# Kernel optimization log

Measured on AMD Instinct MI355X. Metric: run time of the kernel, lower is better.

## Reference

```python
import jax, jax.numpy as jnp
import numpy as np

B, S, DIM, H = 4, 2048, 1024, 16
DEPTH = DIM // H


def setup_inputs() -> dict:
    key = jax.random.key(0)
    ks = jax.random.split(key, 12)
    s = 0.02
    return {
        "Q": jax.random.normal(ks[0], (B, S, DIM), jnp.float32),
        "K": jax.random.normal(ks[1], (B, S, DIM), jnp.float32),
        "V": jax.random.normal(ks[2], (B, S, DIM), jnp.float32),
        "mask": jax.random.randint(ks[3], (B, 1, 1, S), 0, 2).astype(jnp.float32),
        "Wq": jax.random.normal(ks[4], (DIM, DIM), jnp.float32) * s,
        "bq": jnp.zeros((DIM,), jnp.float32),
        "Wk": jax.random.normal(ks[5], (DIM, DIM), jnp.float32) * s,
        "bk": jnp.zeros((DIM,), jnp.float32),
        "Wv": jax.random.normal(ks[6], (DIM, DIM), jnp.float32) * s,
        "bv": jnp.zeros((DIM,), jnp.float32),
        "Wo": jax.random.normal(ks[7], (DIM, DIM), jnp.float32) * s,
        "bo": jnp.zeros((DIM,), jnp.float32),
    }


def _split_heads(x):
    # [B,S,DIM] -> [B,H,S,DEPTH]
    return x.reshape(x.shape[0], x.shape[1], H, DEPTH).transpose(0, 2, 1, 3)


def reference(Q, K, V, mask, Wq, bq, Wk, bk, Wv, bv, Wo, bo):
    q = _split_heads(Q @ Wq + bq)
    k = _split_heads(K @ Wk + bk)
    v = _split_heads(V @ Wv + bv)
    # scaled dot-product attention; note original scales by sqrt(depth) = last dim of K after split
    logits = jnp.einsum("bhqd,bhkd->bhqk", q, k) / jnp.sqrt(jnp.float32(DEPTH))
    logits = logits + mask * -1e9
    attn = jax.nn.softmax(logits, axis=-1)
    ctx = jnp.einsum("bhqk,bhkd->bhqd", attn, v)
    ctx = ctx.transpose(0, 2, 1, 3).reshape(Q.shape[0], Q.shape[1], DIM)
    return ctx @ Wo + bo
```

## Files before the change

### kernel.cpp

```cpp
#include <hip/hip_runtime.h>

typedef short s16x8 __attribute__((ext_vector_type(8)));
typedef short s16x4 __attribute__((ext_vector_type(4)));
typedef float f32x4 __attribute__((ext_vector_type(4)));

#define MFMA32(a, b, c) __builtin_amdgcn_mfma_f32_16x16x32_bf16((a), (b), (c), 0, 0, 0)

#if defined(__HIP_DEVICE_COMPILE__)
#define MFMA16(a, b, c) __builtin_amdgcn_mfma_f32_16x16x16bf16_1k((a), (b), (c), 0, 0, 0)
#else
#define MFMA16(a, b, c) (c)
#endif

__device__ __forceinline__ void stage16(const unsigned short* g, unsigned short* l) {
#if defined(__HIP_DEVICE_COMPILE__)
  __builtin_amdgcn_global_load_lds((const __attribute__((address_space(1))) unsigned int*)g,
                                   (__attribute__((address_space(3))) unsigned int*)l, 16, 0, 0);
#endif
}

__device__ __forceinline__ unsigned short f2b(float f) {
  unsigned int u = __builtin_bit_cast(unsigned int, f);
  unsigned int r = u + 0x7FFFu + ((u >> 16) & 1u);
  return (unsigned short)(r >> 16);
}
__device__ __forceinline__ unsigned int pk2(float a, float b) {
  return (unsigned int)f2b(a) | ((unsigned int)f2b(b) << 16);
}
__device__ __forceinline__ s16x4 mk4(float p0, float p1, float p2, float p3) {
  uint2 u;
  u.x = pk2(p0, p1);
  u.y = pk2(p2, p3);
  return __builtin_bit_cast(s16x4, u);
}
__device__ __forceinline__ float fast_exp2(float x) {
#if defined(__HIP_DEVICE_COMPILE__) && __has_builtin(__builtin_amdgcn_exp2f)
  return __builtin_amdgcn_exp2f(x);
#else
  return exp2f(x);
#endif
}

__global__ void wtrans(const float* __restrict__ W0, const float* __restrict__ W1,
                       const float* __restrict__ W2, const float* __restrict__ W3,
                       unsigned short* __restrict__ T0, unsigned short* __restrict__ T1,
                       unsigned short* __restrict__ T2, unsigned short* __restrict__ T3) {
  const float* W;
  unsigned short* T;
  switch (blockIdx.z) {
    case 0: W = W0; T = T0; break;
    case 1: W = W1; T = T1; break;
    case 2: W = W2; T = T2; break;
    default: W = W3; T = T3; break;
  }
  __shared__ float tile[32][33];
  const int n0 = blockIdx.x << 5;
  const int k0 = blockIdx.y << 5;
  const int tx = threadIdx.x;
  const int ty = threadIdx.y;
#pragma unroll
  for (int j = 0; j < 4; ++j)
    tile[ty + 8 * j][tx] = W[(size_t)(k0 + ty + 8 * j) * 1024 + n0 + tx];
  __syncthreads();
#pragma unroll
  for (int j = 0; j < 4; ++j)
    T[(size_t)(n0 + ty + 8 * j) * 1024 + k0 + tx] = f2b(tile[tx][ty + 8 * j]);
}

template <int MODE>
__global__ __launch_bounds__(256, 2) void gemm_bt(const void* __restrict__ Ain,
                                                  const unsigned short* __restrict__ Bt,
                                                  const float* __restrict__ bias,
                                                  void* __restrict__ Cout, float oscale) {
  __shared__ unsigned short As[128][40];
  __shared__ unsigned short Bs[128][40];
  const int n0 = blockIdx.x * 128;
  const int m0 = blockIdx.y * 128;
  const int tid = threadIdx.x;
  const int srow = tid >> 1;
  const int kc = (tid & 1) << 4;
  const int w = tid >> 6;
  const int lane = tid & 63;
  const int lr = lane & 15;
  const int lg = lane >> 4;
  const int wm = (w >> 1) << 6;
  const int wn = (w & 1) << 6;

  f32x4 acc[4][4];
#pragma unroll
  for (int i = 0; i < 4; ++i)
#pragma unroll
    for (int j = 0; j < 4; ++j) {
      f32x4 z = {0.f, 0.f, 0.f, 0.f};
      acc[i][j] = z;
    }

  const unsigned short* Bp0 = Bt + (size_t)(n0 + srow) * 1024 + kc;

  for (int k0 = 0; k0 < 1024; k0 += 32) {
    if constexpr (MODE != 2) {
      const float* A = (const float*)Ain + (size_t)(m0 + srow) * 1024 + k0 + kc;
      float4 f0 = ((const float4*)A)[0];
      float4 f1 = ((const float4*)A)[1];
      float4 f2 = ((const float4*)A)[2];
      float4 f3 = ((const float4*)A)[3];
      uint4 u0, u1;
      u0.x = pk2(f0.x, f0.y); u0.y = pk2(f0.z, f0.w);
      u0.z = pk2(f1.x, f1.y); u0.w = pk2(f1.z, f1.w);
      u1.x = pk2(f2.x, f2.y); u1.y = pk2(f2.z, f2.w);
      u1.z = pk2(f3.x, f3.y); u1.w = pk2(f3.z, f3.w);
      *(uint4*)&As[srow][kc] = u0;
      *(uint4*)&As[srow][kc + 8] = u1;
    } else {
      const unsigned short* A = (const unsigned short*)Ain + (size_t)(m0 + srow) * 1024 + k0 + kc;
      *(uint4*)&As[srow][kc] = ((const uint4*)A)[0];
      *(uint4*)&As[srow][kc + 8] = ((const uint4*)A)[1];
    }
    {
      const unsigned short* Bp = Bp0 + k0;
      *(uint4*)&Bs[srow][kc] = ((const uint4*)Bp)[0];
      *(uint4*)&Bs[srow][kc + 8] = ((const uint4*)Bp)[1];
    }
    __syncthreads();
    s16x8 af[4], bfr[4];
#pragma unroll
    for (int mt = 0; mt < 4; ++mt) af[mt] = *(const s16x8*)&As[wm + mt * 16 + lr][lg * 8];
#pragma unroll
    for (int nt = 0; nt < 4; ++nt) bfr[nt] = *(const s16x8*)&Bs[wn + nt * 16 + lr][lg * 8];
#pragma unroll
    for (int mt = 0; mt < 4; ++mt)
#pragma unroll
      for (int nt = 0; nt < 4; ++nt)
        acc[mt][nt] = MFMA32(af[mt], bfr[nt], acc[mt][nt]);
    __syncthreads();
  }

  float bcol[4];
#pragma unroll
  for (int nt = 0; nt < 4; ++nt) bcol[nt] = bias[n0 + wn + nt * 16 + lr];

#pragma unroll
  for (int mt = 0; mt < 4; ++mt)
#pragma unroll
    for (int nt = 0; nt < 4; ++nt)
#pragma unroll
      for (int r = 0; r < 4; ++r) {
        float v = (acc[mt][nt][r] + bcol[nt]) * oscale;
        int row = m0 + wm + mt * 16 + lg * 4 + r;
        int col = n0 + wn + nt * 16 + lr;
        if constexpr (MODE == 0) {
          int b = row >> 11, s = row & 2047, hh = col >> 6, d = col & 63;
          ((unsigned short*)Cout)[(((size_t)(b * 16 + hh) * 2048 + s) << 6) + d] = f2b(v);
        } else if constexpr (MODE == 1) {
          int b = row >> 11, s = row & 2047, hh = col >> 6, d = col & 63;
          ((unsigned short*)Cout)[(((size_t)(b * 16 + hh) * 64 + d) << 11) + s] = f2b(v);
        } else {
          ((float*)Cout)[(size_t)row * 1024 + col] = v;
        }
      }
}

__global__ __launch_bounds__(256, 4) void flash_attn(const unsigned short* __restrict__ qh,
                                                     const unsigned short* __restrict__ kh,
                                                     const unsigned short* __restrict__ vt,
                                                     const float* __restrict__ mask,
                                                     unsigned short* __restrict__ ctx) {
  const float c2 = 1.4426950408889634e9f;
  const int id = blockIdx.x;
  const int bh = id & 63;
  const int qtile = id >> 6;
  const int b = bh >> 4;
  const int h = bh & 15;
  const int q0 = qtile << 7;
  const int tid = threadIdx.x;
  const int w = tid >> 6;
  const int lane = tid & 63;
  const int lr = lane & 15;
  const int lg = lane >> 4;

  __shared__ __align__(16) unsigned short Ks[64 * 64];
  __shared__ __align__(16) unsigned short Vs[64 * 64];

  const unsigned short* qbase = qh + ((size_t)bh * 2048 + q0 + w * 32) * 64;
  const unsigned short* kbase = kh + (size_t)bh * 2048 * 64;
  const unsigned short* vbase = vt + (size_t)bh * 64 * 2048;
  const float* mbase = mask + b * 2048;

  const int rowc = lane >> 3;
  const int gseg = (lane & 7) ^ rowc;
  const unsigned short* kg0 = kbase + (size_t)(w * 16 + rowc) * 64 + gseg * 8;
  const unsigned short* kg1 = kbase + (size_t)(w * 16 + 8 + rowc) * 64 + gseg * 8;
  const unsigned short* vg0 = vbase + (size_t)(w * 16 + rowc) * 2048 + gseg * 8;
  const unsigned short* vg1 = vbase + (size_t)(w * 16 + 8 + rowc) * 2048 + gseg * 8;
  unsigned short* kl0 = &Ks[(w * 16 + 0) * 64];
  unsigned short* kl1 = &Ks[(w * 16 + 8) * 64];
  unsigned short* vl0 = &Vs[(w * 16 + 0) * 64];
  unsigned short* vl1 = &Vs[(w * 16 + 8) * 64];

  s16x8 qf[2][2];
#pragma unroll
  for (int qt = 0; qt < 2; ++qt)
#pragma unroll
    for (int kk = 0; kk < 2; ++kk)
      qf[qt][kk] = *(const s16x8*)(qbase + (qt * 16 + lr) * 64 + kk * 32 + lg * 8);

  const s16x4 ones = {(short)0x3F80, (short)0x3F80, (short)0x3F80, (short)0x3F80};

  f32x4 o_acc[2][4];
  f32x4 l_acc[2];
#pragma unroll
  for (int qt = 0; qt < 2; ++qt) {
    f32x4 z = {0.f, 0.f, 0.f, 0.f};
    l_acc[qt] = z;
#pragma unroll
    for (int dt = 0; dt < 4; ++dt) o_acc[qt][dt] = z;
  }

  for (int t0 = 0; t0 < 2048; t0 += 64) {
    stage16(kg0 + (size_t)t0 * 64, kl0);
    stage16(kg1 + (size_t)t0 * 64, kl1);
    stage16(vg0 + t0, vl0);
    stage16(vg1 + t0, vl1);
    float4 mk[4];
#pragma unroll
    for (int kt = 0; kt < 4; ++kt) mk[kt] = *(const float4*)(mbase + t0 + kt * 16 + lg * 4);
    __syncthreads();

    s16x4 pf[4][2];
    const int sw = lr & 7;
#pragma unroll
    for (int kt = 0; kt < 4; ++kt) {
      const int krow = kt * 16 + lr;
      s16x8 kf0 = *(const s16x8*)&Ks[krow * 64 + ((lg ^ sw) * 8)];
      s16x8 kf1 = *(const s16x8*)&Ks[krow * 64 + (((4 + lg) ^ sw) * 8)];
      float ml0 = mk[kt].x * c2, ml1 = mk[kt].y * c2;
      float ml2 = mk[kt].z * c2, ml3 = mk[kt].w * c2;
#pragma unroll
      for (int qt = 0; qt < 2; ++qt) {
        f32x4 s = {0.f, 0.f, 0.f, 0.f};
        s = MFMA32(kf0, qf[qt][0], s);
        s = MFMA32(kf1, qf[qt][1], s);
        pf[kt][qt] = mk4(fast_exp2(s[0] - ml0), fast_exp2(s[1] - ml1),
                         fast_exp2(s[2] - ml2), fast_exp2(s[3] - ml3));
      }
    }

#pragma unroll
    for (int kt = 0; kt < 4; ++kt) {
#pragma unroll
      for (int qt = 0; qt < 2; ++qt) l_acc[qt] = MFMA16(ones, pf[kt][qt], l_acc[qt]);
      const int phys = (kt * 2 + (lg >> 1)) ^ sw;
#pragma unroll
      for (int dt = 0; dt < 4; ++dt) {
        const int d = dt * 16 + lr;
        s16x4 vf = *(const s16x4*)&Vs[d * 64 + phys * 8 + (lg & 1) * 4];
#pragma unroll
        for (int qt = 0; qt < 2; ++qt) o_acc[qt][dt] = MFMA16(vf, pf[kt][qt], o_acc[qt][dt]);
      }
    }
    __syncthreads();
  }

#pragma unroll
  for (int qt = 0; qt < 2; ++qt) {
    float inv = 1.0f / l_acc[qt][0];
    int q = q0 + w * 32 + qt * 16 + lr;
    unsigned short* cp = ctx + ((size_t)(b * 2048 + q) * 16 + h) * 64 + lg * 4;
#pragma unroll
    for (int dt = 0; dt < 4; ++dt) {
      f32x4 o = o_acc[qt][dt];
      uint2 u;
      u.x = pk2(o[0] * inv, o[1] * inv);
      u.y = pk2(o[2] * inv, o[3] * inv);
      *(uint2*)(cp + dt * 16) = u;
    }
  }
}

extern "C" void kernel_launch(void* const* d_in, const int* in_sizes, int n_in,
                              void* d_out, int out_size, void* d_ws, size_t ws_size,
                              hipStream_t stream) {
  (void)in_sizes; (void)n_in; (void)out_size; (void)ws_size;
  const float* Q = (const float*)d_in[0];
  const float* K = (const float*)d_in[1];
  const float* V = (const float*)d_in[2];
  const float* mask = (const float*)d_in[3];
  const float* Wq = (const float*)d_in[4];
  const float* bq = (const float*)d_in[5];
  const float* Wk = (const float*)d_in[6];
  const float* bk = (const float*)d_in[7];
  const float* Wv = (const float*)d_in[8];
  const float* bv = (const float*)d_in[9];
  const float* Wo = (const float*)d_in[10];
  const float* bo = (const float*)d_in[11];

  char* ws = (char*)d_ws;
  unsigned short* wqt = (unsigned short*)(ws + (size_t)0);
  unsigned short* wkt = (unsigned short*)(ws + ((size_t)2 << 20));
  unsigned short* wvt = (unsigned short*)(ws + ((size_t)4 << 20));
  unsigned short* wot = (unsigned short*)(ws + ((size_t)6 << 20));
  unsigned short* qhb = (unsigned short*)(ws + ((size_t)8 << 20));
  unsigned short* khb = (unsigned short*)(ws + ((size_t)24 << 20));
  unsigned short* vtb = (unsigned short*)(ws + ((size_t)40 << 20));
  unsigned short* ctx = (unsigned short*)(ws + ((size_t)56 << 20));

  wtrans<<<dim3(32, 32, 4), dim3(32, 8), 0, stream>>>(Wq, Wk, Wv, Wo, wqt, wkt, wvt, wot);

  const float qscale = 0.18033688011112042f;
  dim3 gg(8, 64), bb(256);
  gemm_bt<0><<<gg, bb, 0, stream>>>(Q, wqt, bq, qhb, qscale);
  gemm_bt<0><<<gg, bb, 0, stream>>>(K, wkt, bk, khb, 1.0f);
  gemm_bt<1><<<gg, bb, 0, stream>>>(V, wvt, bv, vtb, 1.0f);

  flash_attn<<<dim3(1024), dim3(256), 0, stream>>>(qhb, khb, vtb, mask, ctx);

  gemm_bt<2><<<gg, bb, 0, stream>>>(ctx, wot, bo, d_out, 1.0f);
}
```

Baseline: 424.6 us.

## Pre-cast projection inputs to bf16 and stage GEMM tiles via direct global-to-LDS loads

Adds a separate cast kernel that converts Q, K and V from fp32 to bf16 into a scratch buffer before each projection GEMM. The GEMM then always reads bf16 A and stages both operand tiles with global_load_lds straight into unpadded LDS, replacing register round-trips and in-loop conversion. The goal is to cut VGPR staging work and per-iteration conversion in the GEMM main loop. In exchange it adds three extra launches and an extra fp32 read plus bf16 write pass, and dropping the LDS padding may cause bank conflicts on fragment reads.

```diff
diff --git a/kernel.cpp b/kernel.cpp
--- a/kernel.cpp
+++ b/kernel.cpp
@@ -39,6 +39,19 @@
 #else
   return exp2f(x);
 #endif
+}
+
+__global__ __launch_bounds__(256) void castq(const float* __restrict__ X,
+                                             unsigned short* __restrict__ Y) {
+  int i = blockIdx.x * 256 + threadIdx.x;
+  float4 f0 = ((const float4*)X)[i * 2];
+  float4 f1 = ((const float4*)X)[i * 2 + 1];
+  uint4 u;
+  u.x = pk2(f0.x, f0.y);
+  u.y = pk2(f0.z, f0.w);
+  u.z = pk2(f1.x, f1.y);
+  u.w = pk2(f1.z, f1.w);
+  ((uint4*)Y)[i] = u;
 }
 
 __global__ void wtrans(const float* __restrict__ W0, const float* __restrict__ W1,
@@ -68,17 +81,15 @@
 }
 
 template <int MODE>
-__global__ __launch_bounds__(256, 2) void gemm_bt(const void* __restrict__ Ain,
+__global__ __launch_bounds__(256, 2) void gemm_bt(const unsigned short* __restrict__ A,
                                                   const unsigned short* __restrict__ Bt,
                                                   const float* __restrict__ bias,
                                                   void* __restrict__ Cout, float oscale) {
-  __shared__ unsigned short As[128][40];
-  __shared__ unsigned short Bs[128][40];
+  __shared__ __align__(16) unsigned short As[128 * 32];
+  __shared__ __align__(16) unsigned short Bs[128 * 32];
   const int n0 = blockIdx.x * 128;
   const int m0 = blockIdx.y * 128;
   const int tid = threadIdx.x;
-  const int srow = tid >> 1;
-  const int kc = (tid & 1) << 4;
   const int w = tid >> 6;
   const int lane = tid & 63;
   const int lr = lane & 15;
@@ -86,6 +97,17 @@
   const int wm = (w >> 1) << 6;
   const int wn = (w & 1) << 6;
 
+  const int srow = w * 16 + (lane >> 2);
+  const int sseg = lane & 3;
+  const unsigned short* Ag0 = A + (size_t)(m0 + srow) * 1024 + sseg * 8;
+  const unsigned short* Ag1 = A + (size_t)(m0 + 64 + srow) * 1024 + sseg * 8;
+  const unsigned short* Bg0 = Bt + (size_t)(n0 + srow) * 1024 + sseg * 8;
+  const unsigned short* Bg1 = Bt + (size_t)(n0 + 64 + srow) * 1024 + sseg * 8;
+  unsigned short* Al0 = &As[(w * 16) * 32];
+  unsigned short* Al1 = &As[(64 + w * 16) * 32];
+  unsigned short* Bl0 = &Bs[(w * 16) * 32];
+  unsigned short* Bl1 = &Bs[(64 + w * 16) * 32];
+
   f32x4 acc[4][4];
 #pragma unroll
   for (int i = 0; i < 4; ++i)
@@ -95,38 +117,17 @@
       acc[i][j] = z;
     }
 
-  const unsigned short* Bp0 = Bt + (size_t)(n0 + srow) * 1024 + kc;
-
   for (int k0 = 0; k0 < 1024; k0 += 32) {
-    if constexpr (MODE != 2) {
-      const float* A = (const float*)Ain + (size_t)(m0 + srow) * 1024 + k0 + kc;
-      float4 f0 = ((const float4*)A)[0];
-      float4 f1 = ((const float4*)A)[1];
-      float4 f2 = ((const float4*)A)[2];
-      float4 f3 = ((const float4*)A)[3];
-      uint4 u0, u1;
-      u0.x = pk2(f0.x, f0.y); u0.y = pk2(f0.z, f0.w);
-      u0.z = pk2(f1.x, f1.y); u0.w = pk2(f1.z, f1.w);
-      u1.x = pk2(f2.x, f2.y); u1.y = pk2(f2.z, f2.w);
-      u1.z = pk2(f3.x, f3.y); u1.w = pk2(f3.z, f3.w);
-      *(uint4*)&As[srow][kc] = u0;
-      *(uint4*)&As[srow][kc + 8] = u1;
-    } else {
-      const unsigned short* A = (const unsigned short*)Ain + (size_t)(m0 + srow) * 1024 + k0 + kc;
-      *(uint4*)&As[srow][kc] = ((const uint4*)A)[0];
-      *(uint4*)&As[srow][kc + 8] = ((const uint4*)A)[1];
-    }
-    {
-      const unsigned short* Bp = Bp0 + k0;
-      *(uint4*)&Bs[srow][kc] = ((const uint4*)Bp)[0];
-      *(uint4*)&Bs[srow][kc + 8] = ((const uint4*)Bp)[1];
-    }
+    stage16(Ag0 + k0, Al0);
+    stage16(Ag1 + k0, Al1);
+    stage16(Bg0 + k0, Bl0);
+    stage16(Bg1 + k0, Bl1);
     __syncthreads();
     s16x8 af[4], bfr[4];
 #pragma unroll
-    for (int mt = 0; mt < 4; ++mt) af[mt] = *(const s16x8*)&As[wm + mt * 16 + lr][lg * 8];
-#pragma unroll
-    for (int nt = 0; nt < 4; ++nt) bfr[nt] = *(const s16x8*)&Bs[wn + nt * 16 + lr][lg * 8];
+    for (int mt = 0; mt < 4; ++mt) af[mt] = *(const s16x8*)&As[(wm + mt * 16 + lr) * 32 + lg * 8];
+#pragma unroll
+    for (int nt = 0; nt < 4; ++nt) bfr[nt] = *(const s16x8*)&Bs[(wn + nt * 16 + lr) * 32 + lg * 8];
 #pragma unroll
     for (int mt = 0; mt < 4; ++mt)
 #pragma unroll
@@ -302,15 +303,21 @@
   unsigned short* qhb = (unsigned short*)(ws + ((size_t)8 << 20));
   unsigned short* khb = (unsigned short*)(ws + ((size_t)24 << 20));
   unsigned short* vtb = (unsigned short*)(ws + ((size_t)40 << 20));
-  unsigned short* ctx = (unsigned short*)(ws + ((size_t)56 << 20));
+  unsigned short* tmp = (unsigned short*)(ws + ((size_t)56 << 20));
+  unsigned short* ctx = tmp;
 
   wtrans<<<dim3(32, 32, 4), dim3(32, 8), 0, stream>>>(Wq, Wk, Wv, Wo, wqt, wkt, wvt, wot);
 
   const float qscale = 0.18033688011112042f;
   dim3 gg(8, 64), bb(256);
-  gemm_bt<0><<<gg, bb, 0, stream>>>(Q, wqt, bq, qhb, qscale);
-  gemm_bt<0><<<gg, bb, 0, stream>>>(K, wkt, bk, khb, 1.0f);
-  gemm_bt<1><<<gg, bb, 0, stream>>>(V, wvt, bv, vtb, 1.0f);
+  const int castBlocks = (8192 * 1024) / (256 * 8);
+
+  castq<<<castBlocks, 256, 0, stream>>>(Q, tmp);
+  gemm_bt<0><<<gg, bb, 0, stream>>>(tmp, wqt, bq, qhb, qscale);
+  castq<<<castBlocks, 256, 0, stream>>>(K, tmp);
+  gemm_bt<0><<<gg, bb, 0, stream>>>(tmp, wkt, bk, khb, 1.0f);
+  castq<<<castBlocks, 256, 0, stream>>>(V, tmp);
+  gemm_bt<1><<<gg, bb, 0, stream>>>(tmp, wvt, bv, vtb, 1.0f);
 
   flash_attn<<<dim3(1024), dim3(256), 0, stream>>>(qhb, khb, vtb, mask, ctx);
 
```

Measured after the change: 384.4 us. -9.5%, faster.
